# Performance work log

Hardware: AMD Instinct MI355X
Metric: run time of the kernel (lower is better)

Reference implementation:

```python
import jax, jax.numpy as jnp
import numpy as np

N = 50000          # nodes
E = 1250000        # edges (no self loops in raw data)
H = 2              # heads
C = 32             # out channels per head
DIN = 64           # dim_node
ED = 16            # edge_dim
G = 16             # graphs in batch
NC = 5             # num classes
SLOPE = 0.2        # GATConv leaky_relu negative_slope


def _glorot(key, shape):
    fan = shape[0] if len(shape) == 2 else shape[-1]
    return jax.random.normal(key, shape, jnp.float32) * (1.0 / np.sqrt(fan))


def setup_inputs() -> dict:
    key = jax.random.key(0)
    ks = jax.random.split(key, 24)
    x = jax.random.normal(ks[0], (N, DIN), jnp.float32)
    dst = jax.random.randint(ks[1], (E,), 0, N)
    off = jax.random.randint(ks[2], (E,), 1, N)
    src = (dst + off) % N  # guarantees src != dst (PyG removes self loops before re-adding)
    edge_index = jnp.stack([src, dst]).astype(jnp.int32)
    edge_attr = jax.random.normal(ks[3], (E, ED), jnp.float32)
    batch = jnp.sort(jax.random.randint(ks[4], (N,), 0, G)).astype(jnp.int32)
    inp = dict(x=x, edge_index=edge_index, edge_attr=edge_attr, batch=batch)
    # layer 1: in=DIN, heads=H, out=C, concat -> H*C
    inp["W1"] = _glorot(ks[5], (DIN, H * C)); inp["asrc1"] = _glorot(ks[6], (H, C))
    inp["adst1"] = _glorot(ks[7], (H, C)); inp["We1"] = _glorot(ks[8], (ED, H * C))
    inp["ae1"] = _glorot(ks[9], (H, C)); inp["b1"] = jnp.zeros((H * C,), jnp.float32)
    # layer 2: in=H*C, heads=H, out=C, concat
    inp["W2"] = _glorot(ks[10], (H * C, H * C)); inp["asrc2"] = _glorot(ks[11], (H, C))
    inp["adst2"] = _glorot(ks[12], (H, C)); inp["We2"] = _glorot(ks[13], (ED, H * C))
    inp["ae2"] = _glorot(ks[14], (H, C)); inp["b2"] = jnp.zeros((H * C,), jnp.float32)
    # layer 3: in=H*C, heads=1, out=C, concat=False
    inp["W3"] = _glorot(ks[15], (H * C, C)); inp["asrc3"] = _glorot(ks[16], (1, C))
    inp["adst3"] = _glorot(ks[17], (1, C)); inp["We3"] = _glorot(ks[18], (ED, C))
    inp["ae3"] = _glorot(ks[19], (1, C)); inp["b3"] = jnp.zeros((C,), jnp.float32)
    # ffn: Linear(C, NC) + softmax (dropout is identity in eval)
    inp["Wf"] = _glorot(ks[20], (C, NC)); inp["bf"] = jnp.zeros((NC,), jnp.float32)
    return inp


def _gat_layer(h_in, src, dst, eattr, W, asrc, adst, We, ae, b, heads, out, concat):
    n = h_in.shape[0]
    h = (h_in @ W).reshape(n, heads, out)                      # [N,H,C]
    s_src = jnp.einsum('nhc,hc->nh', h, asrc)                  # per-node src scores
    s_dst = jnp.einsum('nhc,hc->nh', h, adst)
    he = (eattr @ We).reshape(-1, heads, out)                  # [E,H,C]
    s_e = jnp.einsum('ehc,hc->eh', he, ae)
    logit = jax.nn.leaky_relu(s_src[src] + s_dst[dst] + s_e, SLOPE)  # [E,H]
    m = jax.ops.segment_max(logit, dst, num_segments=n)
    ex = jnp.exp(logit - m[dst])
    den = jax.ops.segment_sum(ex, dst, num_segments=n)
    alpha = ex / (den[dst] + 1e-16)                            # segment softmax per dst node
    agg = jax.ops.segment_sum(h[src] * alpha[..., None], dst, num_segments=n)  # [N,H,C]
    out_x = agg.reshape(n, heads * out) if concat else agg.mean(axis=1)
    return out_x + b


def _gat_forward(x, edge_index, edge_attr, batch,
                 W1, asrc1, adst1, We1, ae1, b1,
                 W2, asrc2, adst2, We2, ae2, b2,
                 W3, asrc3, adst3, We3, ae3, b3,
                 Wf, bf):
    src, dst = edge_index[0], edge_index[1]
    n = x.shape[0]
    # add_self_loops with fill_value='mean': self-loop edge_attr = mean of incoming edge_attr
    deg = jax.ops.segment_sum(jnp.ones((src.shape[0],), x.dtype), dst, num_segments=n)
    self_attr = jax.ops.segment_sum(edge_attr, dst, num_segments=n) / jnp.maximum(deg, 1.0)[:, None]
    loop = jnp.arange(n, dtype=src.dtype)
    src_a = jnp.concatenate([src, loop])
    dst_a = jnp.concatenate([dst, loop])
    eattr_a = jnp.concatenate([edge_attr, self_attr], axis=0)

    h = jax.nn.relu(_gat_layer(x, src_a, dst_a, eattr_a, W1, asrc1, adst1, We1, ae1, b1, H, C, True))
    h = jax.nn.relu(_gat_layer(h, src_a, dst_a, eattr_a, W2, asrc2, adst2, We2, ae2, b2, H, C, True))
    h = jax.nn.relu(_gat_layer(h, src_a, dst_a, eattr_a, W3, asrc3, adst3, We3, ae3, b3, 1, C, False))

    # global mean pool per graph
    cnt = jax.ops.segment_sum(jnp.ones((n,), h.dtype), batch, num_segments=G)
    pooled = jax.ops.segment_sum(h, batch, num_segments=G) / jnp.maximum(cnt, 1.0)[:, None]
    # ffn: Dropout (identity at eval) -> Linear -> Softmax(dim=1)
    return jax.nn.softmax(pooled @ Wf + bf, axis=1)


def reference(x, edge_index, edge_attr, batch,
              W1, asrc1, adst1, We1, ae1, b1,
              W2, asrc2, adst2, We2, ae2, b2,
              W3, asrc3, adst3, We3, ae3, b3,
              Wf, bf):
    return _gat_forward(x, edge_index, edge_attr, batch,
                        W1, asrc1, adst1, We1, ae1, b1,
                        W2, asrc2, adst2, We2, ae2, b2,
                        W3, asrc3, adst3, We3, ae3, b3,
                        Wf, bf)
```

## Files before the change

kernel.cpp:

```cpp
#include <hip/hip_runtime.h>
#include <math.h>

#define NN 50000
#define EE 1250000
#define GG 16
#define NCLS 5
#define NBIN 391
#define BINSHIFT 7
#define CAPB 3900
#define NABLK 153
#define NTBLK 3125

constexpr size_t AL(size_t x){ return (x + 255) & ~size_t(255); }
constexpr size_t OFF_ROWPTR = 0;
constexpr size_t OFF_SRCS   = OFF_ROWPTR + AL((size_t)(NN+1)*4);
constexpr size_t OFF_SE12   = OFF_SRCS + AL((size_t)EE*2);
constexpr size_t OFF_SE34   = OFF_SE12 + AL((size_t)EE*4);
constexpr size_t OFF_SE5    = OFF_SE34 + AL((size_t)EE*4);
constexpr size_t OFF_SSRC   = OFF_SE5 + AL((size_t)EE*2);
constexpr size_t OFF_SDST   = OFF_SSRC + AL((size_t)NN*2*4);
constexpr size_t OFF_STAG   = OFF_SDST + AL((size_t)NN*2*4);
constexpr size_t OFF_BUFH   = OFF_STAG + AL((size_t)NBIN*CAPB*16);
constexpr size_t OFF_BUFO   = OFF_BUFH + AL((size_t)NN*32*4);
constexpr size_t OFF_POOL   = OFF_BUFO + AL((size_t)NN*64*4);

__device__ __forceinline__ float leaky(float x){ return x > 0.f ? x : 0.2f*x; }
__device__ __forceinline__ unsigned rne_bf16(float x){
    unsigned u = __float_as_uint(x);
    return (u + 0x7FFFu + ((u >> 16) & 1u)) >> 16;
}
__device__ __forceinline__ float bf16lo(unsigned p){ return __uint_as_float(p << 16); }
__device__ __forceinline__ float bf16hi(unsigned p){ return __uint_as_float(p & 0xFFFF0000u); }

__global__ __launch_bounds__(1024)
void binAt1_kernel(const int* __restrict__ src, const int* __restrict__ dst,
                   const float* __restrict__ eattr,
                   const float* __restrict__ We1, const float* __restrict__ ae1,
                   const float* __restrict__ We2, const float* __restrict__ ae2,
                   const float* __restrict__ We3, const float* __restrict__ ae3,
                   int* __restrict__ bincursor, int4* __restrict__ staging,
                   const float* __restrict__ x, const float* __restrict__ W1,
                   const float* __restrict__ asrc1, const float* __restrict__ adst1,
                   unsigned* __restrict__ hout2, float* __restrict__ ssrc,
                   float* __restrict__ sdst, int nE, int nN){
    __shared__ float smem[5120];
    int tid = threadIdx.x;

    if (blockIdx.x >= NABLK){
        float* Ws  = smem;
        float* ins = smem + 4096;
        for (int i = tid; i < 4096; i += 1024) Ws[i] = W1[i];
        int base = (blockIdx.x - NABLK) * 16;
        {
            int n = base + (tid >> 6);
            ins[tid] = (n < nN) ? x[(size_t)n*64 + (tid & 63)] : 0.f;
        }
        __syncthreads();
        int r = tid >> 6, c = tid & 63;
        int n = base + r;
        float acc = 0.f;
        #pragma unroll
        for (int d = 0; d < 64; ++d) acc += ins[r*64 + d] * Ws[d*64 + c];
        float ps = acc * asrc1[c];
        float pd = acc * adst1[c];
        #pragma unroll
        for (int m = 1; m <= 16; m <<= 1){ ps += __shfl_xor(ps, m); pd += __shfl_xor(pd, m); }
        float accN = __shfl_xor(acc, 1);
        if (n < nN){
            if ((c & 1) == 0){
                unsigned pk = rne_bf16(acc) | (rne_bf16(accN) << 16);
                hout2[(size_t)n*32 + (c >> 1)] = pk;
            }
            if ((c & 31) == 0){
                int h = c >> 5;
                ssrc[n*2 + h] = ps;
                sdst[n*2 + h] = pd;
            }
        }
        return;
    }

    int*   lcount = (int*)smem;
    int*   lbase  = lcount + NBIN;
    float* w      = (float*)(lbase + NBIN);
    if (tid < 80){
        int j = tid >> 4, d = tid & 15;
        const float* We; const float* ae; int hc, h;
        if (j == 0){ We = We1; ae = ae1; hc = 64; h = 0; }
        else if (j == 1){ We = We1; ae = ae1; hc = 64; h = 1; }
        else if (j == 2){ We = We2; ae = ae2; hc = 64; h = 0; }
        else if (j == 3){ We = We2; ae = ae2; hc = 64; h = 1; }
        else { We = We3; ae = ae3; hc = 32; h = 0; }
        float s = 0.f;
        for (int c = 0; c < 32; ++c) s += We[d*hc + h*32 + c] * ae[h*32 + c];
        w[tid] = s;
    }
    for (int i = tid; i < NBIN; i += 1024) lcount[i] = 0;
    __syncthreads();
    int base = blockIdx.x * 8192;
    int w0[8], bn[8], idx[8]; unsigned p01[8], p23[8], p4[8];
    #pragma unroll
    for (int k = 0; k < 8; ++k){
        int i = base + k*1024 + tid;
        if (i < nE){
            int d = dst[i];
            int s = src[i];
            bn[k]  = d >> BINSHIFT;
            w0[k]  = s | ((d & 127) << 16);
            const float4* row = (const float4*)(eattr + (size_t)i*16);
            float4 a0 = row[0], a1 = row[1], a2 = row[2], a3 = row[3];
            float a[16] = {a0.x,a0.y,a0.z,a0.w, a1.x,a1.y,a1.z,a1.w,
                           a2.x,a2.y,a2.z,a2.w, a3.x,a3.y,a3.z,a3.w};
            float sj[5];
            #pragma unroll
            for (int j = 0; j < 5; ++j){
                float s2 = 0.f;
                #pragma unroll
                for (int d2 = 0; d2 < 16; ++d2) s2 += a[d2]*w[j*16+d2];
                sj[j] = s2;
            }
            p01[k] = rne_bf16(sj[0]) | (rne_bf16(sj[1]) << 16);
            p23[k] = rne_bf16(sj[2]) | (rne_bf16(sj[3]) << 16);
            p4[k]  = rne_bf16(sj[4]);
            idx[k] = atomicAdd(&lcount[bn[k]], 1);
        } else bn[k] = -1;
    }
    __syncthreads();
    for (int i = tid; i < NBIN; i += 1024){
        int c = lcount[i];
        lbase[i] = c ? (i*CAPB + atomicAdd(&bincursor[i], c)) : 0;
    }
    __syncthreads();
    #pragma unroll
    for (int k = 0; k < 8; ++k)
        if (bn[k] >= 0)
            staging[lbase[bn[k]] + idx[k]] = make_int4(w0[k], (int)p01[k], (int)p23[k], (int)p4[k]);
}

__global__ void binB_kernel(const int* __restrict__ bincursor, const int4* __restrict__ staging,
                            unsigned short* __restrict__ srcs, unsigned* __restrict__ se12,
                            unsigned* __restrict__ se34, unsigned short* __restrict__ se5,
                            int* __restrict__ rowptr, int nN){
    __shared__ int4 lout[CAPB];
    __shared__ int lcnt[128];
    __shared__ int lpre[128];
    __shared__ int sbb;
    int b = blockIdx.x;
    int sbase = b*CAPB;
    int cnt = bincursor[b];
    int tid = threadIdx.x;
    if (tid < 128) lcnt[tid] = 0;
    if (tid < 64){
        int sum = 0;
        for (int i = tid; i < b; i += 64) sum += bincursor[i];
        #pragma unroll
        for (int m = 1; m < 64; m <<= 1) sum += __shfl_xor(sum, m);
        if (tid == 0) sbb = sum;
    }
    __syncthreads();
    for (int k = tid; k < cnt; k += 1024)
        atomicAdd(&lcnt[staging[sbase + k].x >> 16], 1);
    __syncthreads();
    if (tid < 64){
        int a0 = lcnt[2*tid], a1 = lcnt[2*tid+1];
        int pair = a0 + a1, incl = pair;
        #pragma unroll
        for (int off = 1; off < 64; off <<= 1){
            int t = __shfl_up(incl, off);
            if (tid >= off) incl += t;
        }
        int base0 = incl - pair;
        lpre[2*tid] = base0;
        lpre[2*tid+1] = base0 + a0;
    }
    __syncthreads();
    int r0 = sbb;
    int lo = b << BINSHIFT;
    if (tid < 128 && lo + tid < nN) rowptr[lo + tid] = r0 + lpre[tid];
    if (b == 0 && tid == 0) rowptr[nN] = EE;
    if (tid < 128) lcnt[tid] = 0;
    __syncthreads();
    for (int k = tid; k < cnt; k += 1024){
        int4 v = staging[sbase + k];
        int dl = v.x >> 16;
        int rank = atomicAdd(&lcnt[dl], 1);
        v.x &= 0xFFFF;
        lout[lpre[dl] + rank] = v;
    }
    __syncthreads();
    for (int k = tid; k < cnt; k += 1024){
        int4 v = lout[k];
        srcs[r0 + k] = (unsigned short)v.x;
        se12[r0 + k] = (unsigned)v.y;
        se34[r0 + k] = (unsigned)v.z;
        se5[r0 + k]  = (unsigned short)v.w;
    }
}

template<int OUTC>
__global__ void transform_kernel(const float* __restrict__ in, const float* __restrict__ W,
                                 const float* __restrict__ asrc, const float* __restrict__ adst,
                                 unsigned* __restrict__ hout2, float* __restrict__ ssrc,
                                 float* __restrict__ sdst, int nN){
    constexpr int R = 256/OUTC;
    __shared__ float Ws[64*OUTC];
    __shared__ float ins[R*64];
    int tid = threadIdx.x;
    for (int i = tid; i < 64*OUTC; i += 256) Ws[i] = W[i];
    int base = blockIdx.x * R;
    for (int i = tid; i < R*64; i += 256){
        int n = base + i/64;
        ins[i] = (n < nN) ? in[(size_t)n*64 + (i & 63)] : 0.f;
    }
    __syncthreads();
    int r = tid / OUTC, c = tid % OUTC;
    int n = base + r;
    float acc = 0.f;
    #pragma unroll
    for (int d = 0; d < 64; ++d) acc += ins[r*64 + d] * Ws[d*OUTC + c];
    float ps = acc * asrc[c];
    float pd = acc * adst[c];
    #pragma unroll
    for (int m = 1; m <= 16; m <<= 1){ ps += __shfl_xor(ps, m); pd += __shfl_xor(pd, m); }
    float accN = __shfl_xor(acc, 1);
    if (n < nN){
        if ((c & 1) == 0){
            unsigned pk = rne_bf16(acc) | (rne_bf16(accN) << 16);
            hout2[(size_t)n*(OUTC/2) + (c >> 1)] = pk;
        }
        constexpr int HEADS = OUTC/32;
        if ((c & 31) == 0){
            int h = c >> 5;
            ssrc[n*HEADS + h] = ps;
            sdst[n*HEADS + h] = pd;
        }
    }
}

template<int OUTC>
__global__ void agg_kernel(const int* __restrict__ rowptr, const unsigned short* __restrict__ srcs,
                           const unsigned* __restrict__ sePa, const unsigned short* __restrict__ sePb,
                           const float* __restrict__ ssrc, const float* __restrict__ sdst,
                           const unsigned* __restrict__ hbuf2, const float* __restrict__ bias,
                           float* __restrict__ outbuf, int nN){
    constexpr int HEADS = OUTC/32;
    constexpr int HALF  = OUTC/4;
    constexpr int EPI   = 64/HALF;
    int wid = threadIdx.x >> 6;
    int lane = threadIdx.x & 63;
    int n = blockIdx.x*4 + wid;
    if (n >= nN) return;
    int row_start = rowptr[n], row_end = rowptr[n+1];
    int degn = row_end - row_start;
    float sd0 = sdst[n*HEADS + 0];
    float sd1 = (HEADS == 2) ? sdst[n*HEADS + 1] : 0.f;

    int sub = lane / HALF;
    int lc  = lane & (HALF - 1);
    int h   = (HEADS == 2) ? ((4*lc) >> 5) : 0;

    float acc0=0.f, acc1=0.f, acc2=0.f, acc3=0.f, den=0.f;
    float ssp0=0.f, ssp1=0.f;
    const uint2* hb2 = (const uint2*)hbuf2;

    for (int p0 = row_start; p0 < row_end; p0 += 64){
        int myp = p0 + lane;
        int srcreg = 0; unsigned wpk = 0; float w0s = 0.f;
        if (myp < row_end){
            srcreg = srcs[myp];
            if (HEADS == 2){
                unsigned pk = sePa[myp];
                float e0 = bf16lo(pk);
                float e1 = bf16hi(pk);
                ssp0 += e0; ssp1 += e1;
                float2 sv = ((const float2*)ssrc)[srcreg];
                float w0 = __expf(leaky(sv.x + sd0 + e0));
                float w1 = __expf(leaky(sv.y + sd1 + e1));
                wpk = rne_bf16(w0) | (rne_bf16(w1) << 16);
            } else {
                float e0 = __uint_as_float(((unsigned)sePb[myp]) << 16);
                ssp0 += e0;
                w0s = __expf(leaky(ssrc[srcreg] + sd0 + e0));
            }
        }
        int cnt = min(64, row_end - p0);
        #pragma unroll 4
        for (int q = sub; q < cnt; q += EPI){
            int sj = __shfl(srcreg, q);
            float wj;
            if (HEADS == 2){
                unsigned wq = __shfl(wpk, q);
                wj = h ? bf16hi(wq) : bf16lo(wq);
            } else {
                wj = __shfl(w0s, q);
            }
            den += wj;
            uint2 hv = hb2[(size_t)sj*(OUTC/4) + lc];
            acc0 += wj * bf16lo(hv.x);
            acc1 += wj * bf16hi(hv.x);
            acc2 += wj * bf16lo(hv.y);
            acc3 += wj * bf16hi(hv.y);
        }
    }

    #pragma unroll
    for (int m = HALF; m < 64; m <<= 1){
        acc0 += __shfl_xor(acc0, m); acc1 += __shfl_xor(acc1, m);
        acc2 += __shfl_xor(acc2, m); acc3 += __shfl_xor(acc3, m);
        den  += __shfl_xor(den, m);
    }
    #pragma unroll
    for (int m = 1; m < 64; m <<= 1){
        ssp0 += __shfl_xor(ssp0, m);
        if (HEADS == 2) ssp1 += __shfl_xor(ssp1, m);
    }

    float invdeg = 1.f / (float)max(degn, 1);
    float srh = ssrc[n*HEADS + h];
    float sdh = h ? sd1 : sd0;
    float ssh = h ? ssp1 : ssp0;
    float wself = __expf(leaky(srh + sdh + ssh*invdeg));
    uint2 hv = hb2[(size_t)n*(OUTC/4) + lc];
    acc0 += wself * bf16lo(hv.x); acc1 += wself * bf16hi(hv.x);
    acc2 += wself * bf16lo(hv.y); acc3 += wself * bf16hi(hv.y);
    den += wself;

    if (lane < HALF){
        float inv = 1.f / (den + 1e-16f);
        float4 o;
        o.x = fmaxf(acc0*inv + bias[4*lc+0], 0.f);
        o.y = fmaxf(acc1*inv + bias[4*lc+1], 0.f);
        o.z = fmaxf(acc2*inv + bias[4*lc+2], 0.f);
        o.w = fmaxf(acc3*inv + bias[4*lc+3], 0.f);
        ((float4*)outbuf)[(size_t)n*(OUTC/4) + lc] = o;
    }
}

__global__ void pool_kernel(const float* __restrict__ h3, const int* __restrict__ batch,
                            float* __restrict__ pool, float* __restrict__ cnt, int nN){
    __shared__ float accs[GG*32];
    __shared__ float acccnt[GG];
    int tid = threadIdx.x;
    for (int i = tid; i < GG*32; i += 256) accs[i] = 0.f;
    if (tid < GG) acccnt[tid] = 0.f;
    __syncthreads();
    int r = tid >> 5, c = tid & 31;
    int base = blockIdx.x * 512;
    int end = min(base + 512, nN);
    for (int n = base + r; n < end; n += 8){
        int g = batch[n];
        atomicAdd(&accs[g*32 + c], h3[(size_t)n*32 + c]);
        if (c == 0) atomicAdd(&acccnt[g], 1.f);
    }
    __syncthreads();
    for (int i = tid; i < GG*32; i += 256) atomicAdd(&pool[i], accs[i]);
    if (tid < GG) atomicAdd(&cnt[tid], acccnt[tid]);
}

__global__ void final_kernel(const float* __restrict__ pool, const float* __restrict__ cnt,
                             const float* __restrict__ Wf, const float* __restrict__ bf,
                             float* __restrict__ out){
    int g = threadIdx.x;
    if (g >= GG) return;
    float ic = 1.f / fmaxf(cnt[g], 1.f);
    float lg[NCLS];
    #pragma unroll
    for (int k = 0; k < NCLS; ++k) lg[k] = bf[k];
    for (int c = 0; c < 32; ++c){
        float v = pool[g*32 + c] * ic;
        #pragma unroll
        for (int k = 0; k < NCLS; ++k) lg[k] += v * Wf[c*NCLS + k];
    }
    float mx = lg[0];
    #pragma unroll
    for (int k = 1; k < NCLS; ++k) mx = fmaxf(mx, lg[k]);
    float sum = 0.f, ex[NCLS];
    #pragma unroll
    for (int k = 0; k < NCLS; ++k){ ex[k] = expf(lg[k] - mx); sum += ex[k]; }
    #pragma unroll
    for (int k = 0; k < NCLS; ++k) out[g*NCLS + k] = ex[k]/sum;
}

extern "C" void kernel_launch(void* const* d_in, const int* in_sizes, int n_in,
                              void* d_out, int out_size, void* d_ws, size_t ws_size,
                              hipStream_t stream){
    const float* x     = (const float*)d_in[0];
    const int*   eidx  = (const int*)d_in[1];
    const float* eattr = (const float*)d_in[2];
    const int*   batch = (const int*)d_in[3];
    const float* W1 = (const float*)d_in[4];  const float* asrc1 = (const float*)d_in[5];
    const float* adst1 = (const float*)d_in[6]; const float* We1 = (const float*)d_in[7];
    const float* ae1 = (const float*)d_in[8];  const float* b1 = (const float*)d_in[9];
    const float* W2 = (const float*)d_in[10]; const float* asrc2 = (const float*)d_in[11];
    const float* adst2 = (const float*)d_in[12]; const float* We2 = (const float*)d_in[13];
    const float* ae2 = (const float*)d_in[14]; const float* b2 = (const float*)d_in[15];
    const float* W3 = (const float*)d_in[16]; const float* asrc3 = (const float*)d_in[17];
    const float* adst3 = (const float*)d_in[18]; const float* We3 = (const float*)d_in[19];
    const float* ae3 = (const float*)d_in[20]; const float* b3 = (const float*)d_in[21];
    const float* Wf = (const float*)d_in[22]; const float* bf = (const float*)d_in[23];
    float* out = (float*)d_out;

    char* ws = (char*)d_ws;
    int*   rowptr = (int*)(ws + OFF_ROWPTR);
    unsigned short* srcs = (unsigned short*)(ws + OFF_SRCS);
    unsigned* se12 = (unsigned*)(ws + OFF_SE12);
    unsigned* se34 = (unsigned*)(ws + OFF_SE34);
    unsigned short* se5 = (unsigned short*)(ws + OFF_SE5);
    float* ssrc   = (float*)(ws + OFF_SSRC);
    float* sdst   = (float*)(ws + OFF_SDST);
    int4*  staging = (int4*)(ws + OFF_STAG);
    unsigned* bufH = (unsigned*)(ws + OFF_BUFH);
    float* bufO   = (float*)(ws + OFF_BUFO);
    float* pool   = (float*)(ws + OFF_POOL);
    float* cnt    = pool + GG*32;
    int*   bincursor = (int*)(cnt + GG);

    const int* srcA = eidx;
    const int* dstA = eidx + EE;

    hipMemsetAsync(pool, 0, (GG*32 + GG)*4 + NBIN*4, stream);

    binAt1_kernel<<<NABLK + NTBLK, 1024, 0, stream>>>(srcA, dstA, eattr,
                                                      We1, ae1, We2, ae2, We3, ae3,
                                                      bincursor, staging,
                                                      x, W1, asrc1, adst1,
                                                      bufH, ssrc, sdst, EE, NN);
    binB_kernel<<<NBIN, 1024, 0, stream>>>(bincursor, staging, srcs, se12, se34, se5, rowptr, NN);

    int ngrid4 = (NN + 3)/4;
    int ngrid8 = (NN + 7)/8;
    agg_kernel<64><<<ngrid4, 256, 0, stream>>>(rowptr, srcs, se12, nullptr,
                                               ssrc, sdst, bufH, b1, bufO, NN);
    transform_kernel<64><<<ngrid4, 256, 0, stream>>>(bufO, W2, asrc2, adst2, bufH, ssrc, sdst, NN);
    agg_kernel<64><<<ngrid4, 256, 0, stream>>>(rowptr, srcs, se34, nullptr,
                                               ssrc, sdst, bufH, b2, bufO, NN);
    transform_kernel<32><<<ngrid8, 256, 0, stream>>>(bufO, W3, asrc3, adst3, bufH, ssrc, sdst, NN);
    agg_kernel<32><<<ngrid4, 256, 0, stream>>>(rowptr, srcs, nullptr, se5,
                                               ssrc, sdst, bufH, b3, bufO, NN);
    pool_kernel<<<(NN + 511)/512, 256, 0, stream>>>(bufO, batch, pool, cnt, NN);
    final_kernel<<<1, 64, 0, stream>>>(pool, cnt, Wf, bf, out);
}
```

Measured before the change: 260.2 us.

## Fuse next-layer linear transform into aggregation epilogue with ping-pong buffers

The separate transform kernels are removed. Each 64-channel aggregation block now keeps its 16 per-node results in shared memory and applies the next layer's weight matrix and attention projections directly, writing the bf16 features and scores for the next layer. Ping-pong buffers avoid overwriting data that other nodes still read. This drops the fp32 intermediate write and read between aggregate and transform, plus two launches. In exchange it uses 1024-thread blocks with a block barrier, so work-imbalanced waves wait on the slowest node.

New measurement: 257.4 us (median of 2 runs). Within noise of the previous version (-1.1%).

```diff
diff --git a/kernel.cpp b/kernel.cpp
--- a/kernel.cpp
+++ b/kernel.cpp
@@ -17,12 +17,15 @@
 constexpr size_t OFF_SE12   = OFF_SRCS + AL((size_t)EE*2);
 constexpr size_t OFF_SE34   = OFF_SE12 + AL((size_t)EE*4);
 constexpr size_t OFF_SE5    = OFF_SE34 + AL((size_t)EE*4);
-constexpr size_t OFF_SSRC   = OFF_SE5 + AL((size_t)EE*2);
-constexpr size_t OFF_SDST   = OFF_SSRC + AL((size_t)NN*2*4);
-constexpr size_t OFF_STAG   = OFF_SDST + AL((size_t)NN*2*4);
-constexpr size_t OFF_BUFH   = OFF_STAG + AL((size_t)NBIN*CAPB*16);
-constexpr size_t OFF_BUFO   = OFF_BUFH + AL((size_t)NN*32*4);
-constexpr size_t OFF_POOL   = OFF_BUFO + AL((size_t)NN*64*4);
+constexpr size_t OFF_SSRCA  = OFF_SE5 + AL((size_t)EE*2);
+constexpr size_t OFF_SDSTA  = OFF_SSRCA + AL((size_t)NN*2*4);
+constexpr size_t OFF_SSRCB  = OFF_SDSTA + AL((size_t)NN*2*4);
+constexpr size_t OFF_SDSTB  = OFF_SSRCB + AL((size_t)NN*2*4);
+constexpr size_t OFF_STAG   = OFF_SDSTB + AL((size_t)NN*2*4);
+constexpr size_t OFF_BUFHA  = OFF_STAG + AL((size_t)NBIN*CAPB*16);
+constexpr size_t OFF_BUFHB  = OFF_BUFHA + AL((size_t)NN*32*4);
+constexpr size_t OFF_BUFO   = OFF_BUFHB + AL((size_t)NN*32*4);
+constexpr size_t OFF_POOL   = OFF_BUFO + AL((size_t)NN*32*4);
 
 __device__ __forceinline__ float leaky(float x){ return x > 0.f ? x : 0.2f*x; }
 __device__ __forceinline__ unsigned rne_bf16(float x){
@@ -197,142 +200,190 @@
     }
 }
 
-template<int OUTC>
-__global__ void transform_kernel(const float* __restrict__ in, const float* __restrict__ W,
-                                 const float* __restrict__ asrc, const float* __restrict__ adst,
-                                 unsigned* __restrict__ hout2, float* __restrict__ ssrc,
-                                 float* __restrict__ sdst, int nN){
-    constexpr int R = 256/OUTC;
-    __shared__ float Ws[64*OUTC];
-    __shared__ float ins[R*64];
+template<int NEXTC>
+__global__ __launch_bounds__(1024)
+void agg64f_kernel(const int* __restrict__ rowptr, const unsigned short* __restrict__ srcs,
+                   const unsigned* __restrict__ sePa,
+                   const float* __restrict__ ssrc, const float* __restrict__ sdst,
+                   const unsigned* __restrict__ hbuf2, const float* __restrict__ bias,
+                   const float* __restrict__ Wn, const float* __restrict__ asrcn,
+                   const float* __restrict__ adstn,
+                   unsigned* __restrict__ houtn, float* __restrict__ ssrcn,
+                   float* __restrict__ sdstn, int nN){
+    __shared__ float WnS[64*NEXTC];
+    __shared__ float os[16*64];
     int tid = threadIdx.x;
-    for (int i = tid; i < 64*OUTC; i += 256) Ws[i] = W[i];
-    int base = blockIdx.x * R;
-    for (int i = tid; i < R*64; i += 256){
-        int n = base + i/64;
-        ins[i] = (n < nN) ? in[(size_t)n*64 + (i & 63)] : 0.f;
-    }
-    __syncthreads();
-    int r = tid / OUTC, c = tid % OUTC;
-    int n = base + r;
-    float acc = 0.f;
-    #pragma unroll
-    for (int d = 0; d < 64; ++d) acc += ins[r*64 + d] * Ws[d*OUTC + c];
-    float ps = acc * asrc[c];
-    float pd = acc * adst[c];
-    #pragma unroll
-    for (int m = 1; m <= 16; m <<= 1){ ps += __shfl_xor(ps, m); pd += __shfl_xor(pd, m); }
-    float accN = __shfl_xor(acc, 1);
-    if (n < nN){
+    int wid = tid >> 6;
+    int lane = tid & 63;
+    for (int i = tid; i < 64*NEXTC; i += 1024) WnS[i] = Wn[i];
+    int n = blockIdx.x*16 + wid;
+
+    int row_start = rowptr[n], row_end = rowptr[n+1];
+    int degn = row_end - row_start;
+    float sd0 = sdst[n*2 + 0];
+    float sd1 = sdst[n*2 + 1];
+    int sub = lane >> 4;
+    int lc  = lane & 15;
+    int h   = lc >> 3;
+    float acc0=0.f, acc1=0.f, acc2=0.f, acc3=0.f, den=0.f;
+    float ssp0=0.f, ssp1=0.f;
+    const uint2* hb2 = (const uint2*)hbuf2;
+
+    for (int p0 = row_start; p0 < row_end; p0 += 64){
+        int myp = p0 + lane;
+        int srcreg = 0; unsigned wpk = 0;
+        if (myp < row_end){
+            srcreg = srcs[myp];
+            unsigned pk = sePa[myp];
+            float e0 = bf16lo(pk);
+            float e1 = bf16hi(pk);
+            ssp0 += e0; ssp1 += e1;
+            float2 sv = ((const float2*)ssrc)[srcreg];
+            float w0 = __expf(leaky(sv.x + sd0 + e0));
+            float w1 = __expf(leaky(sv.y + sd1 + e1));
+            wpk = rne_bf16(w0) | (rne_bf16(w1) << 16);
+        }
+        int cnt = min(64, row_end - p0);
+        #pragma unroll 4
+        for (int q = sub; q < cnt; q += 4){
+            int sj = __shfl(srcreg, q);
+            unsigned wq = __shfl(wpk, q);
+            float wj = h ? bf16hi(wq) : bf16lo(wq);
+            den += wj;
+            uint2 hv = hb2[(size_t)sj*16 + lc];
+            acc0 += wj * bf16lo(hv.x);
+            acc1 += wj * bf16hi(hv.x);
+            acc2 += wj * bf16lo(hv.y);
+            acc3 += wj * bf16hi(hv.y);
+        }
+    }
+    #pragma unroll
+    for (int m = 16; m < 64; m <<= 1){
+        acc0 += __shfl_xor(acc0, m); acc1 += __shfl_xor(acc1, m);
+        acc2 += __shfl_xor(acc2, m); acc3 += __shfl_xor(acc3, m);
+        den  += __shfl_xor(den, m);
+    }
+    #pragma unroll
+    for (int m = 1; m < 64; m <<= 1){
+        ssp0 += __shfl_xor(ssp0, m);
+        ssp1 += __shfl_xor(ssp1, m);
+    }
+    float invdeg = 1.f / (float)max(degn, 1);
+    float srh = ssrc[n*2 + h];
+    float sdh = h ? sd1 : sd0;
+    float ssh = h ? ssp1 : ssp0;
+    float wself = __expf(leaky(srh + sdh + ssh*invdeg));
+    uint2 hv = hb2[(size_t)n*16 + lc];
+    acc0 += wself * bf16lo(hv.x); acc1 += wself * bf16hi(hv.x);
+    acc2 += wself * bf16lo(hv.y); acc3 += wself * bf16hi(hv.y);
+    den += wself;
+    if (lane < 16){
+        float inv = 1.f / (den + 1e-16f);
+        os[wid*64 + 4*lc+0] = fmaxf(acc0*inv + bias[4*lc+0], 0.f);
+        os[wid*64 + 4*lc+1] = fmaxf(acc1*inv + bias[4*lc+1], 0.f);
+        os[wid*64 + 4*lc+2] = fmaxf(acc2*inv + bias[4*lc+2], 0.f);
+        os[wid*64 + 4*lc+3] = fmaxf(acc3*inv + bias[4*lc+3], 0.f);
+    }
+    __syncthreads();
+    if (NEXTC == 64){
+        int c = lane;
+        float hh = 0.f;
+        #pragma unroll
+        for (int d = 0; d < 64; ++d) hh += os[wid*64 + d] * WnS[d*64 + c];
+        float ps = hh * asrcn[c];
+        float pd = hh * adstn[c];
+        #pragma unroll
+        for (int m = 1; m <= 16; m <<= 1){ ps += __shfl_xor(ps, m); pd += __shfl_xor(pd, m); }
+        float hN = __shfl_xor(hh, 1);
         if ((c & 1) == 0){
-            unsigned pk = rne_bf16(acc) | (rne_bf16(accN) << 16);
-            hout2[(size_t)n*(OUTC/2) + (c >> 1)] = pk;
-        }
-        constexpr int HEADS = OUTC/32;
+            unsigned pk = rne_bf16(hh) | (rne_bf16(hN) << 16);
+            houtn[(size_t)n*32 + (c >> 1)] = pk;
+        }
         if ((c & 31) == 0){
-            int h = c >> 5;
-            ssrc[n*HEADS + h] = ps;
-            sdst[n*HEADS + h] = pd;
-        }
-    }
-}
-
-template<int OUTC>
-__global__ void agg_kernel(const int* __restrict__ rowptr, const unsigned short* __restrict__ srcs,
-                           const unsigned* __restrict__ sePa, const unsigned short* __restrict__ sePb,
-                           const float* __restrict__ ssrc, const float* __restrict__ sdst,
-                           const unsigned* __restrict__ hbuf2, const float* __restrict__ bias,
-                           float* __restrict__ outbuf, int nN){
-    constexpr int HEADS = OUTC/32;
-    constexpr int HALF  = OUTC/4;
-    constexpr int EPI   = 64/HALF;
+            int hh2 = c >> 5;
+            ssrcn[n*2 + hh2] = ps;
+            sdstn[n*2 + hh2] = pd;
+        }
+    } else {
+        int c = lane & 31, dh = lane >> 5;
+        float part = 0.f;
+        #pragma unroll
+        for (int d = 0; d < 32; ++d) part += os[wid*64 + dh*32 + d] * WnS[(dh*32 + d)*32 + c];
+        float hh = part + __shfl_xor(part, 32);
+        float ps = hh * asrcn[c];
+        float pd = hh * adstn[c];
+        #pragma unroll
+        for (int m = 1; m <= 16; m <<= 1){ ps += __shfl_xor(ps, m); pd += __shfl_xor(pd, m); }
+        float hN = __shfl_xor(hh, 1);
+        if (lane < 32 && (c & 1) == 0){
+            unsigned pk = rne_bf16(hh) | (rne_bf16(hN) << 16);
+            houtn[(size_t)n*16 + (c >> 1)] = pk;
+        }
+        if (lane == 0){ ssrcn[n] = ps; sdstn[n] = pd; }
+    }
+}
+
+__global__ void agg32_kernel(const int* __restrict__ rowptr, const unsigned short* __restrict__ srcs,
+                             const unsigned short* __restrict__ sePb,
+                             const float* __restrict__ ssrc, const float* __restrict__ sdst,
+                             const unsigned* __restrict__ hbuf2, const float* __restrict__ bias,
+                             float* __restrict__ outbuf, int nN){
     int wid = threadIdx.x >> 6;
     int lane = threadIdx.x & 63;
     int n = blockIdx.x*4 + wid;
     if (n >= nN) return;
     int row_start = rowptr[n], row_end = rowptr[n+1];
     int degn = row_end - row_start;
-    float sd0 = sdst[n*HEADS + 0];
-    float sd1 = (HEADS == 2) ? sdst[n*HEADS + 1] : 0.f;
-
-    int sub = lane / HALF;
-    int lc  = lane & (HALF - 1);
-    int h   = (HEADS == 2) ? ((4*lc) >> 5) : 0;
-
-    float acc0=0.f, acc1=0.f, acc2=0.f, acc3=0.f, den=0.f;
-    float ssp0=0.f, ssp1=0.f;
+    float sd0 = sdst[n];
+    int sub = lane >> 3;
+    int lc  = lane & 7;
+    float acc0=0.f, acc1=0.f, acc2=0.f, acc3=0.f, den=0.f, ssp0=0.f;
     const uint2* hb2 = (const uint2*)hbuf2;
 
     for (int p0 = row_start; p0 < row_end; p0 += 64){
         int myp = p0 + lane;
-        int srcreg = 0; unsigned wpk = 0; float w0s = 0.f;
+        int srcreg = 0; float w0s = 0.f;
         if (myp < row_end){
             srcreg = srcs[myp];
-            if (HEADS == 2){
-                unsigned pk = sePa[myp];
-                float e0 = bf16lo(pk);
-                float e1 = bf16hi(pk);
-                ssp0 += e0; ssp1 += e1;
-                float2 sv = ((const float2*)ssrc)[srcreg];
-                float w0 = __expf(leaky(sv.x + sd0 + e0));
-                float w1 = __expf(leaky(sv.y + sd1 + e1));
-                wpk = rne_bf16(w0) | (rne_bf16(w1) << 16);
-            } else {
-                float e0 = __uint_as_float(((unsigned)sePb[myp]) << 16);
-                ssp0 += e0;
-                w0s = __expf(leaky(ssrc[srcreg] + sd0 + e0));
-            }
+            float e0 = __uint_as_float(((unsigned)sePb[myp]) << 16);
+            ssp0 += e0;
+            w0s = __expf(leaky(ssrc[srcreg] + sd0 + e0));
         }
         int cnt = min(64, row_end - p0);
         #pragma unroll 4
-        for (int q = sub; q < cnt; q += EPI){
+        for (int q = sub; q < cnt; q += 8){
             int sj = __shfl(srcreg, q);
-            float wj;
-            if (HEADS == 2){
-                unsigned wq = __shfl(wpk, q);
-                wj = h ? bf16hi(wq) : bf16lo(wq);
-            } else {
-                wj = __shfl(w0s, q);
-            }
+            float wj = __shfl(w0s, q);
             den += wj;
-            uint2 hv = hb2[(size_t)sj*(OUTC/4) + lc];
+            uint2 hv = hb2[(size_t)sj*8 + lc];
             acc0 += wj * bf16lo(hv.x);
             acc1 += wj * bf16hi(hv.x);
             acc2 += wj * bf16lo(hv.y);
             acc3 += wj * bf16hi(hv.y);
         }
     }
-
-    #pragma unroll
-    for (int m = HALF; m < 64; m <<= 1){
+    #pragma unroll
+    for (int m = 8; m < 64; m <<= 1){
         acc0 += __shfl_xor(acc0, m); acc1 += __shfl_xor(acc1, m);
         acc2 += __shfl_xor(acc2, m); acc3 += __shfl_xor(acc3, m);
         den  += __shfl_xor(den, m);
     }
     #pragma unroll
-    for (int m = 1; m < 64; m <<= 1){
-        ssp0 += __shfl_xor(ssp0, m);
-        if (HEADS == 2) ssp1 += __shfl_xor(ssp1, m);
-    }
-
+    for (int m = 1; m < 64; m <<= 1) ssp0 += __shfl_xor(ssp0, m);
     float invdeg = 1.f / (float)max(degn, 1);
-    float srh = ssrc[n*HEADS + h];
-    float sdh = h ? sd1 : sd0;
-    float ssh = h ? ssp1 : ssp0;
-    float wself = __expf(leaky(srh + sdh + ssh*invdeg));
-    uint2 hv = hb2[(size_t)n*(OUTC/4) + lc];
+    float wself = __expf(leaky(ssrc[n] + sd0 + ssp0*invdeg));
+    uint2 hv = hb2[(size_t)n*8 + lc];
     acc0 += wself * bf16lo(hv.x); acc1 += wself * bf16hi(hv.x);
     acc2 += wself * bf16lo(hv.y); acc3 += wself * bf16hi(hv.y);
     den += wself;
-
-    if (lane < HALF){
+    if (lane < 8){
         float inv = 1.f / (den + 1e-16f);
         float4 o;
         o.x = fmaxf(acc0*inv + bias[4*lc+0], 0.f);
         o.y = fmaxf(acc1*inv + bias[4*lc+1], 0.f);
         o.z = fmaxf(acc2*inv + bias[4*lc+2], 0.f);
         o.w = fmaxf(acc3*inv + bias[4*lc+3], 0.f);
-        ((float4*)outbuf)[(size_t)n*(OUTC/4) + lc] = o;
+        ((float4*)outbuf)[(size_t)n*8 + lc] = o;
     }
 }
 
@@ -406,10 +457,13 @@
     unsigned* se12 = (unsigned*)(ws + OFF_SE12);
     unsigned* se34 = (unsigned*)(ws + OFF_SE34);
     unsigned short* se5 = (unsigned short*)(ws + OFF_SE5);
-    float* ssrc   = (float*)(ws + OFF_SSRC);
-    float* sdst   = (float*)(ws + OFF_SDST);
+    float* ssrcA  = (float*)(ws + OFF_SSRCA);
+    float* sdstA  = (float*)(ws + OFF_SDSTA);
+    float* ssrcB  = (float*)(ws + OFF_SSRCB);
+    float* sdstB  = (float*)(ws + OFF_SDSTB);
     int4*  staging = (int4*)(ws + OFF_STAG);
-    unsigned* bufH = (unsigned*)(ws + OFF_BUFH);
+    unsigned* bufHA = (unsigned*)(ws + OFF_BUFHA);
+    unsigned* bufHB = (unsigned*)(ws + OFF_BUFHB);
     float* bufO   = (float*)(ws + OFF_BUFO);
     float* pool   = (float*)(ws + OFF_POOL);
     float* cnt    = pool + GG*32;
@@ -424,19 +478,17 @@
                                                       We1, ae1, We2, ae2, We3, ae3,
                                                       bincursor, staging,
                                                       x, W1, asrc1, adst1,
-                                                      bufH, ssrc, sdst, EE, NN);
+                                                      bufHA, ssrcA, sdstA, EE, NN);
     binB_kernel<<<NBIN, 1024, 0, stream>>>(bincursor, staging, srcs, se12, se34, se5, rowptr, NN);
 
-    int ngrid4 = (NN + 3)/4;
-    int ngrid8 = (NN + 7)/8;
-    agg_kernel<64><<<ngrid4, 256, 0, stream>>>(rowptr, srcs, se12, nullptr,
-                                               ssrc, sdst, bufH, b1, bufO, NN);
-    transform_kernel<64><<<ngrid4, 256, 0, stream>>>(bufO, W2, asrc2, adst2, bufH, ssrc, sdst, NN);
-    agg_kernel<64><<<ngrid4, 256, 0, stream>>>(rowptr, srcs, se34, nullptr,
-                                               ssrc, sdst, bufH, b2, bufO, NN);
-    transform_kernel<32><<<ngrid8, 256, 0, stream>>>(bufO, W3, asrc3, adst3, bufH, ssrc, sdst, NN);
-    agg_kernel<32><<<ngrid4, 256, 0, stream>>>(rowptr, srcs, nullptr, se5,
-                                               ssrc, sdst, bufH, b3, bufO, NN);
+    agg64f_kernel<64><<<NTBLK, 1024, 0, stream>>>(rowptr, srcs, se12, ssrcA, sdstA,
+                                                  bufHA, b1, W2, asrc2, adst2,
+                                                  bufHB, ssrcB, sdstB, NN);
+    agg64f_kernel<32><<<NTBLK, 1024, 0, stream>>>(rowptr, srcs, se34, ssrcB, sdstB,
+                                                  bufHB, b2, W3, asrc3, adst3,
+                                                  bufHA, ssrcA, sdstA, NN);
+    agg32_kernel<<<(NN + 3)/4, 256, 0, stream>>>(rowptr, srcs, se5, ssrcA, sdstA,
+                                                 bufHA, b3, bufO, NN);
     pool_kernel<<<(NN + 511)/512, 256, 0, stream>>>(bufO, batch, pool, cnt, NN);
     final_kernel<<<1, 64, 0, stream>>>(pool, cnt, Wf, bf, out);
 }
```
